# Kernel tuning notes

Measured on AMD Instinct MI355X. Metric: run time of the kernel, lower is better.

Reference implementation:

```python
import jax, jax.numpy as jnp
import numpy as np

D_MODEL = 1024
HEADS = 16
HEAD_DIM = D_MODEL // HEADS


def setup_inputs() -> dict:
    key = jax.random.key(0)
    ks = jax.random.split(key, 9)
    s = 1.0 / np.sqrt(D_MODEL)
    inp = {
        "inputs": jax.random.normal(ks[0], (4, 2048, D_MODEL), dtype=jnp.float32),
        "Wq": jax.random.normal(ks[1], (D_MODEL, D_MODEL), dtype=jnp.float32) * s,
        "bq": jnp.zeros((D_MODEL,), dtype=jnp.float32),
        "Wk": jax.random.normal(ks[2], (D_MODEL, D_MODEL), dtype=jnp.float32) * s,
        "bk": jnp.zeros((D_MODEL,), dtype=jnp.float32),
        "Wv": jax.random.normal(ks[3], (D_MODEL, D_MODEL), dtype=jnp.float32) * s,
        "bv": jnp.zeros((D_MODEL,), dtype=jnp.float32),
        "Wo": jax.random.normal(ks[4], (D_MODEL, D_MODEL), dtype=jnp.float32) * s,
        "bo": jnp.zeros((D_MODEL,), dtype=jnp.float32),
    }
    return inp


def reference(inputs, Wq, bq, Wk, bk, Wv, bv, Wo, bo):
    bs, seq, _ = inputs.shape
    # projections -> [b, h, s, d]
    def split_heads(x):
        return x.reshape(bs, seq, HEADS, HEAD_DIM).transpose(0, 2, 1, 3)
    q = split_heads(inputs @ Wq + bq)
    k = split_heads(inputs @ Wk + bk)
    v = split_heads(inputs @ Wv + bv)
    # NOTE: original code divides by (head_dim ** 1 / 2) == head_dim/2, not sqrt(head_dim)
    scale = HEAD_DIM / 2.0
    scores = jnp.einsum("bhqd,bhkd->bhqk", q, k) / scale
    attn = jax.nn.softmax(scores, axis=-1)
    out = jnp.einsum("bhqk,bhkd->bhqd", attn, v)
    out = out.transpose(0, 2, 1, 3).reshape(bs, seq, HEADS * HEAD_DIM)
    return out @ Wo + bo
```

## Files before the change

kernel.cpp:

```cpp
#include <hip/hip_runtime.h>
#include <stdint.h>

typedef __attribute__((ext_vector_type(8))) short bf16x8;
typedef __attribute__((ext_vector_type(4))) float f32x4;
typedef __attribute__((address_space(1))) void as1_void;
typedef __attribute__((address_space(3))) void as3_void;

#define D_MODEL 1024
#define SEQ     2048
#define BATCH   4
#define HEADS   16
#define HDIM    64

#define QSCALE 0.045084220029218407f

__device__ __forceinline__ ushort f2bf(float f) {
  union { float f; unsigned u; } v; v.f = f;
  unsigned u = v.u + 0x7fffu + ((v.u >> 16) & 1u);
  return (ushort)(u >> 16);
}

__device__ __forceinline__ void gload_lds16(const void* g, void* l) {
  __builtin_amdgcn_global_load_lds((as1_void*)(uintptr_t)g, (as3_void*)l, 16, 0, 0);
}

__device__ __forceinline__ bf16x8 pack8(float a0, float a1, float a2, float a3,
                                        float a4, float a5, float a6, float a7) {
  union { uint u[4]; bf16x8 v; } x;
  x.u[0] = __builtin_amdgcn_perm(__float_as_uint(a1), __float_as_uint(a0), 0x07060302);
  x.u[1] = __builtin_amdgcn_perm(__float_as_uint(a3), __float_as_uint(a2), 0x07060302);
  x.u[2] = __builtin_amdgcn_perm(__float_as_uint(a5), __float_as_uint(a4), 0x07060302);
  x.u[3] = __builtin_amdgcn_perm(__float_as_uint(a7), __float_as_uint(a6), 0x07060302);
  return x.v;
}

__global__ void prep_kernel(const float* __restrict__ X,
                            const float* w0, const float* w1, const float* w2, const float* w3,
                            const float* __restrict__ bq, const float* __restrict__ bk,
                            const float* __restrict__ bv,
                            ushort* __restrict__ Xb, ushort* __restrict__ WT,
                            float* __restrict__ bcat) {
  __shared__ float tile[32][33];
  const int bx = blockIdx.x, t = threadIdx.x;
  if (bx < 8192) {
    int i = bx * 256 + t;
    float4 f = reinterpret_cast<const float4*>(X)[i];
    ushort4 o;
    o.x = f2bf(f.x); o.y = f2bf(f.y); o.z = f2bf(f.z); o.w = f2bf(f.w);
    reinterpret_cast<ushort4*>(Xb)[i] = o;
  } else if (bx < 12288) {
    int tz = bx - 8192;
    int z = tz >> 10;
    int xy = tz & 1023;
    int bxt = xy & 31, byt = xy >> 5;
    const float* w = (z == 0) ? w0 : (z == 1) ? w1 : (z == 2) ? w2 : w3;
    const float sc = (z == 0) ? QSCALE : 1.0f;
    ushort* o = WT + (size_t)z * D_MODEL * D_MODEL;
    int tx = t & 31, ty = t >> 5;
    int x = bxt * 32 + tx;
    int y0 = byt * 32;
    #pragma unroll
    for (int i = ty; i < 32; i += 8)
      tile[i][tx] = w[(size_t)(y0 + i) * D_MODEL + x];
    __syncthreads();
    #pragma unroll
    for (int i = ty; i < 32; i += 8)
      o[(size_t)(bxt * 32 + i) * D_MODEL + y0 + tx] = f2bf(tile[tx][i] * sc);
  } else {
    int i = (bx - 12288) * 256 + t;
    bcat[i] = (i < 1024) ? bq[i] * QSCALE : (i < 2048) ? bk[i - 1024] : bv[i - 2048];
  }
}

#define MFMA16(a, b, c) __builtin_amdgcn_mfma_f32_16x16x32_bf16(a, b, c, 0, 0, 0)

template <int BN, bool F32OUT>
__global__ __launch_bounds__(256, 2) void gemm2p(const ushort* __restrict__ A,
                                                 const ushort* __restrict__ BT,
                                                 const float* __restrict__ bias,
                                                 ushort* __restrict__ QK,
                                                 ushort* __restrict__ Vt,
                                                 float* __restrict__ Cf) {
  static_assert(BN == 128, "gemm2p tuned for BN=128");
  constexpr int BB = BN * 128;
  __shared__ __align__(16) char smem[32768 + 2 * BB];
  const int tid  = threadIdx.x;
  const int w    = tid >> 6, lane = tid & 63;
  const int lo   = lane & 15, quad = lane >> 4;
  const int wr   = w >> 1, wc = w & 1;

  const int nx   = gridDim.x;
  const int nwg  = nx * gridDim.y;
  const int orig = blockIdx.y * nx + blockIdx.x;
  const int wg   = (orig & 7) * (nwg >> 3) + (orig >> 3);
  const int m0   = (wg / nx) * 128;
  const int n0   = (wg % nx) * BN;

  const int tl = tid ^ ((tid >> 3) & 7);
  const ushort* sA = A  + (size_t)(m0 + (tl >> 3)) * 1024 + (tl & 7) * 8;
  const ushort* sB = BT + (size_t)(n0 + (tl >> 3)) * 1024 + (tl & 7) * 8;
  char* lwA = smem + w * 1024;
  char* lwB = smem + 32768 + w * 1024;

  const int o0 = (quad * 16) ^ ((lo & 7) << 4);
  const int o1 = o0 ^ 64;
  const int rdA = (wr * 64 + lo) * 128;
  const int rdB = 32768 + (wc * 64 + lo) * 128;

  f32x4 acc[4][4];
  #pragma unroll
  for (int i = 0; i < 4; ++i)
    #pragma unroll
    for (int j = 0; j < 4; ++j) acc[i][j] = {0.f, 0.f, 0.f, 0.f};

  gload_lds16(sA,             lwA);
  gload_lds16(sA + 32 * 1024, lwA + 4096);
  gload_lds16(sA + 64 * 1024, lwA + 8192);
  gload_lds16(sA + 96 * 1024, lwA + 12288);
  gload_lds16(sB,             lwB);
  gload_lds16(sB + 64 * 1024, lwB + 8192);
  gload_lds16(sB + 32 * 1024, lwB + 4096);
  gload_lds16(sB + 96 * 1024, lwB + 12288);
  asm volatile("s_waitcnt vmcnt(2)" ::: "memory");
  __builtin_amdgcn_s_barrier();
  asm volatile("" ::: "memory");

  const char* L = smem;
  #pragma unroll 2
  for (int kt = 0; kt < 16; ++kt) {
    const int bA = (kt & 1) << 14;
    const int bB = (kt & 1) * BB;
    const int nA = bA ^ 16384;
    const int nB = bB ^ BB;
    const int kc = (kt + 1) * 64;
    const bool pf = kt < 15;
    bf16x8 af[4][2], bfr[2][2];

    #pragma unroll
    for (int mi = 0; mi < 4; ++mi) {
      af[mi][0] = *(const bf16x8*)(L + bA + rdA + mi * 2048 + o0);
      af[mi][1] = *(const bf16x8*)(L + bA + rdA + mi * 2048 + o1);
    }
    #pragma unroll
    for (int j = 0; j < 2; ++j) {
      bfr[j][0] = *(const bf16x8*)(L + bB + rdB + j * 2048 + o0);
      bfr[j][1] = *(const bf16x8*)(L + bB + rdB + j * 2048 + o1);
    }
    if (pf) {
      gload_lds16(sA + kc,             lwA + nA);
      gload_lds16(sA + 32 * 1024 + kc, lwA + nA + 4096);
      gload_lds16(sA + 64 * 1024 + kc, lwA + nA + 8192);
      gload_lds16(sA + 96 * 1024 + kc, lwA + nA + 12288);
      gload_lds16(sB + kc,             lwB + nB);
      gload_lds16(sB + 64 * 1024 + kc, lwB + nB + 8192);
    }
    asm volatile("s_waitcnt lgkmcnt(0)" ::: "memory");
    __builtin_amdgcn_sched_barrier(0);
    __builtin_amdgcn_s_setprio(1);
    #pragma unroll
    for (int ks = 0; ks < 2; ++ks)
      #pragma unroll
      for (int mi = 0; mi < 4; ++mi) {
        acc[mi][0] = MFMA16(af[mi][ks], bfr[0][ks], acc[mi][0]);
        acc[mi][1] = MFMA16(af[mi][ks], bfr[1][ks], acc[mi][1]);
      }
    __builtin_amdgcn_s_setprio(0);
    if (pf) asm volatile("s_waitcnt vmcnt(6)" ::: "memory");
    else    asm volatile("s_waitcnt vmcnt(0)" ::: "memory");
    __builtin_amdgcn_s_barrier();
    asm volatile("" ::: "memory");

    #pragma unroll
    for (int j = 0; j < 2; ++j) {
      bfr[j][0] = *(const bf16x8*)(L + bB + rdB + (2 + j) * 2048 + o0);
      bfr[j][1] = *(const bf16x8*)(L + bB + rdB + (2 + j) * 2048 + o1);
    }
    if (pf) {
      gload_lds16(sB + 32 * 1024 + kc, lwB + nB + 4096);
      gload_lds16(sB + 96 * 1024 + kc, lwB + nB + 12288);
    }
    asm volatile("s_waitcnt lgkmcnt(0)" ::: "memory");
    __builtin_amdgcn_sched_barrier(0);
    __builtin_amdgcn_s_setprio(1);
    #pragma unroll
    for (int ks = 0; ks < 2; ++ks)
      #pragma unroll
      for (int mi = 0; mi < 4; ++mi) {
        acc[mi][2] = MFMA16(af[mi][ks], bfr[0][ks], acc[mi][2]);
        acc[mi][3] = MFMA16(af[mi][ks], bfr[1][ks], acc[mi][3]);
      }
    __builtin_amdgcn_s_setprio(0);
    if (pf) {
      asm volatile("s_waitcnt vmcnt(2)" ::: "memory");
      __builtin_amdgcn_s_barrier();
      asm volatile("" ::: "memory");
    }
  }

  if constexpr (F32OUT) {
    #pragma unroll
    for (int ni = 0; ni < 4; ++ni) {
      const int col = n0 + wc * 64 + ni * 16 + lo;
      const float bv = bias[col];
      #pragma unroll
      for (int mi = 0; mi < 4; ++mi) {
        const int row = m0 + wr * 64 + mi * 16 + quad * 4;
        #pragma unroll
        for (int r = 0; r < 4; ++r)
          Cf[(size_t)(row + r) * 1024 + col] = acc[mi][ni][r] + bv;
      }
    }
  } else if (n0 < 2048) {
    #pragma unroll
    for (int ni = 0; ni < 4; ++ni) {
      const int col = n0 + wc * 64 + ni * 16 + lo;
      const float bv = bias[col];
      #pragma unroll
      for (int mi = 0; mi < 4; ++mi) {
        const int row = m0 + wr * 64 + mi * 16 + quad * 4;
        #pragma unroll
        for (int r = 0; r < 4; ++r)
          QK[(size_t)(row + r) * 2048 + col] = f2bf(acc[mi][ni][r] + bv);
      }
    }
  } else {
    #pragma unroll
    for (int ni = 0; ni < 4; ++ni) {
      const int col  = n0 + wc * 64 + ni * 16 + lo;
      const int vcol = col - 2048;
      const int hh = vcol >> 6, d = vcol & 63;
      const float bv = bias[col];
      #pragma unroll
      for (int mi = 0; mi < 4; ++mi) {
        const int base = m0 + wr * 64 + mi * 16;
        const int brow = base + quad * 4;
        const int bidx = brow >> 11;
        const int srow = brow & 2047;
        const int ck   = srow >> 6;
        const int c0   = (base & 32) + (quad << 3) + ((base >> 2) & 4);
        ushort e0 = f2bf(acc[mi][ni][0] + bv);
        ushort e1 = f2bf(acc[mi][ni][1] + bv);
        ushort e2 = f2bf(acc[mi][ni][2] + bv);
        ushort e3 = f2bf(acc[mi][ni][3] + bv);
        uint2 pk;
        pk.x = (uint)e0 | ((uint)e1 << 16);
        pk.y = (uint)e2 | ((uint)e3 << 16);
        *(uint2*)&Vt[(size_t)((bidx * HEADS + hh) * HDIM + d) * SEQ + ck * 64 + c0] = pk;
      }
    }
  }
}

__global__ __launch_bounds__(256, 2) void attn_kernel(const ushort* __restrict__ QK,
                                                      const ushort* __restrict__ Vt,
                                                      ushort* __restrict__ Og) {
  __shared__ __align__(16) ushort Ks[2][128 * 64];
  __shared__ __align__(16) ushort Vs[2][64 * 128];

  const int tid  = threadIdx.x;
  const int w    = tid >> 6, lane = tid & 63;
  const int lo   = lane & 15, quad = lane >> 4;

  const int p  = blockIdx.x + (blockIdx.y << 3) + (blockIdx.z << 7);
  const int G  = ((p >> 6) << 3) | (p & 7);
  const int h  = G & 15, b = G >> 4;
  const int qbase = ((p >> 3) & 7) * 256 + w * 64;
  const int swz = lo & 7;

  auto STAGE = [&](int buf, int ck) {
    #pragma unroll
    for (int i = 0; i < 4; ++i) {
      const int seg = w * 4 + i;
      const int c16 = seg * 64 + lane;
      const int rK = c16 >> 3, pK = c16 & 7;
      const int gK = pK ^ (rK & 7);
      gload_lds16(QK + (size_t)(b * SEQ + ck * 128 + rK) * 2048 + 1024 + h * HDIM + gK * 8,
                  &Ks[buf][seg * 512]);
      const int rV = c16 >> 4, pV = c16 & 15;
      const int gV = pV ^ (rV & 7);
      gload_lds16(Vt + (size_t)((b * HEADS + h) * HDIM + rV) * SEQ + ck * 128 + gV * 8,
                  &Vs[buf][seg * 512]);
    }
  };

  bf16x8 qf[4][2];
  #pragma unroll
  for (int qg = 0; qg < 4; ++qg) {
    const ushort* qp = QK + (size_t)(b * SEQ + qbase + qg * 16 + lo) * 2048 + h * HDIM;
    qf[qg][0] = *(const bf16x8*)(qp + quad * 8);
    qf[qg][1] = *(const bf16x8*)(qp + 32 + quad * 8);
  }

  bf16x8 ones;
  { union { uint u[4]; bf16x8 v; } o;
    o.u[0] = o.u[1] = o.u[2] = o.u[3] = 0x3F803F80u; ones = o.v; }

  f32x4 acc[4][4], acc_l[4];
  #pragma unroll
  for (int qg = 0; qg < 4; ++qg) {
    acc_l[qg] = {0.f, 0.f, 0.f, 0.f};
    #pragma unroll
    for (int t = 0; t < 4; ++t) acc[qg][t] = {0.f, 0.f, 0.f, 0.f};
  }

  STAGE(0, 0);
  __syncthreads();

  #pragma unroll 2
  for (int ck = 0; ck < SEQ / 128; ++ck) {
    const int cur = ck & 1;
    if (ck < SEQ / 128 - 1) {
      STAGE(cur ^ 1, ck + 1);
      asm volatile("s_waitcnt vmcnt(8)" ::: "memory");
    } else {
      asm volatile("s_waitcnt vmcnt(0)" ::: "memory");
    }
    __builtin_amdgcn_s_barrier();
    asm volatile("" ::: "memory");

    bf16x8 af[4][4];
    #pragma unroll
    for (int half = 0; half < 2; ++half) {
      bf16x8 kf[4][2];
      #pragma unroll
      for (int s2 = 0; s2 < 4; ++s2) {
        const ushort* kr = &Ks[cur][((half * 4 + s2) * 16 + lo) * 64];
        kf[s2][0] = *(const bf16x8*)(kr + ((quad ^ swz) * 8));
        kf[s2][1] = *(const bf16x8*)(kr + (((4 + quad) ^ swz) * 8));
      }
      #pragma unroll
      for (int qg = 0; qg < 4; ++qg) {
        f32x4 s[4];
        #pragma unroll
        for (int s2 = 0; s2 < 4; ++s2) s[s2] = {0.f, 0.f, 0.f, 0.f};
        #pragma unroll
        for (int s2 = 0; s2 < 4; ++s2) {
          s[s2] = MFMA16(kf[s2][0], qf[qg][0], s[s2]);
          s[s2] = MFMA16(kf[s2][1], qf[qg][1], s[s2]);
        }
        float p2[4][4];
        #pragma unroll
        for (int s2 = 0; s2 < 4; ++s2)
          #pragma unroll
          for (int r = 0; r < 4; ++r) p2[s2][r] = __builtin_amdgcn_exp2f(s[s2][r]);
        af[qg][half * 2 + 0] = pack8(p2[0][0], p2[0][1], p2[0][2], p2[0][3],
                                     p2[1][0], p2[1][1], p2[1][2], p2[1][3]);
        af[qg][half * 2 + 1] = pack8(p2[2][0], p2[2][1], p2[2][2], p2[2][3],
                                     p2[3][0], p2[3][1], p2[3][2], p2[3][3]);
      }
    }

    __builtin_amdgcn_s_setprio(1);
    #pragma unroll
    for (int qg = 0; qg < 4; ++qg)
      #pragma unroll
      for (int hh = 0; hh < 4; ++hh)
        acc_l[qg] = MFMA16(af[qg][hh], ones, acc_l[qg]);
    #pragma unroll
    for (int t = 0; t < 4; ++t) {
      const ushort* vr = &Vs[cur][(t * 16 + lo) * 128];
      #pragma unroll
      for (int hh = 0; hh < 4; ++hh) {
        bf16x8 vf = *(const bf16x8*)(vr + (((hh * 4 + quad) ^ swz) * 8));
        #pragma unroll
        for (int qg = 0; qg < 4; ++qg)
          acc[qg][t] = MFMA16(af[qg][hh], vf, acc[qg][t]);
      }
    }
    __builtin_amdgcn_s_setprio(0);

    asm volatile("" ::: "memory");
    __builtin_amdgcn_s_barrier();
    asm volatile("" ::: "memory");
  }

  #pragma unroll
  for (int qg = 0; qg < 4; ++qg) {
    float linv[4];
    #pragma unroll
    for (int r = 0; r < 4; ++r) linv[r] = 1.0f / acc_l[qg][r];
    #pragma unroll
    for (int t = 0; t < 4; ++t)
      #pragma unroll
      for (int r = 0; r < 4; ++r)
        Og[(size_t)(b * SEQ + qbase + qg * 16 + quad * 4 + r) * D_MODEL + h * HDIM + t * 16 + lo] =
            f2bf(acc[qg][t][r] * linv[r]);
  }
}

extern "C" void kernel_launch(void* const* d_in, const int* in_sizes, int n_in,
                              void* d_out, int out_size, void* d_ws, size_t ws_size,
                              hipStream_t stream) {
  const float* X  = (const float*)d_in[0];
  const float* Wq = (const float*)d_in[1];
  const float* bq = (const float*)d_in[2];
  const float* Wk = (const float*)d_in[3];
  const float* bk = (const float*)d_in[4];
  const float* Wv = (const float*)d_in[5];
  const float* bv = (const float*)d_in[6];
  const float* Wo = (const float*)d_in[7];
  const float* bo = (const float*)d_in[8];
  float* out = (float*)d_out;
  char* ws = (char*)d_ws;

  ushort* Xb  = (ushort*)(ws);
  ushort* WT  = (ushort*)(ws + 16777216);
  ushort* QKb = (ushort*)(ws + 25165824);
  ushort* Vtb = (ushort*)(ws + 58720256);
  ushort* Ob  = (ushort*)(ws + 75497472);
  float*  bcat = (float*)(ws + 75497472);
  const int WSTRIDE = D_MODEL * D_MODEL;

  prep_kernel<<<12300, 256, 0, stream>>>(X, Wq, Wk, Wv, Wo, bq, bk, bv, Xb, WT, bcat);

  gemm2p<128, false><<<dim3(24, 64), 256, 0, stream>>>(Xb, WT, bcat, QKb, Vtb, nullptr);

  attn_kernel<<<dim3(SEQ / 256, HEADS, BATCH), 256, 0, stream>>>(QKb, Vtb, Ob);

  gemm2p<128, true><<<dim3(8, 64), 256, 0, stream>>>(Ob, WT + 3 * WSTRIDE, bo, nullptr, nullptr, out);
}
```

Measured before the change: 241.2 us.

## Software-pipeline attention halves so PV of previous half overlaps next QK/exp

Splits each 128-key chunk of the attention loop into two 64-key halves and interleaves them across iterations. The P·V MFMAs of the previous chunk's second half run alongside the QK and exp2 work of the current chunk, so exp/VALU work can overlap matrix work. V is staged into three rotating 64x64-half buffers so the delayed PV still has its data. The change adds LDS use (K double buffer plus a V triple buffer), a prologue and epilogue, drops the setprio hints and the unroll-2 pragma, and may raise register pressure.

Measured after the change: 252.1 us. 4.6% more time.

```diff
diff --git a/kernel.cpp b/kernel.cpp
--- a/kernel.cpp
+++ b/kernel.cpp
@@ -254,8 +254,8 @@
 __global__ __launch_bounds__(256, 2) void attn_kernel(const ushort* __restrict__ QK,
                                                       const ushort* __restrict__ Vt,
                                                       ushort* __restrict__ Og) {
-  __shared__ __align__(16) ushort Ks[2][128 * 64];
-  __shared__ __align__(16) ushort Vs[2][64 * 128];
+  __shared__ __align__(16) ushort KsL[2 * 128 * 64];
+  __shared__ __align__(16) ushort VsL[3 * 2 * 64 * 64];
 
   const int tid  = threadIdx.x;
   const int w    = tid >> 6, lane = tid & 63;
@@ -267,7 +267,7 @@
   const int qbase = ((p >> 3) & 7) * 256 + w * 64;
   const int swz = lo & 7;
 
-  auto STAGE = [&](int buf, int ck) {
+  auto STAGE = [&](int kb, int vb, int ck) {
     #pragma unroll
     for (int i = 0; i < 4; ++i) {
       const int seg = w * 4 + i;
@@ -275,11 +275,13 @@
       const int rK = c16 >> 3, pK = c16 & 7;
       const int gK = pK ^ (rK & 7);
       gload_lds16(QK + (size_t)(b * SEQ + ck * 128 + rK) * 2048 + 1024 + h * HDIM + gK * 8,
-                  &Ks[buf][seg * 512]);
-      const int rV = c16 >> 4, pV = c16 & 15;
-      const int gV = pV ^ (rV & 7);
-      gload_lds16(Vt + (size_t)((b * HEADS + h) * HDIM + rV) * SEQ + ck * 128 + gV * 8,
-                  &Vs[buf][seg * 512]);
+                  &KsL[kb * 8192 + seg * 512]);
+      const int half = seg >> 3;
+      const int d = (seg & 7) * 8 + (lane >> 3);
+      const int pV = lane & 7;
+      const int gV = pV ^ (d & 7);
+      gload_lds16(Vt + (size_t)((b * HEADS + h) * HDIM + d) * SEQ + ck * 128 + half * 64 + gV * 8,
+                  &VsL[vb * 8192 + seg * 512]);
     }
   };
 
@@ -303,14 +305,78 @@
     for (int t = 0; t < 4; ++t) acc[qg][t] = {0.f, 0.f, 0.f, 0.f};
   }
 
-  STAGE(0, 0);
+  auto HALF = [&](bf16x8 (&afo)[4][2], int kb, int half) {
+    const ushort* kbase = &KsL[kb * 8192];
+    bf16x8 kf[4][2];
+    #pragma unroll
+    for (int s2 = 0; s2 < 4; ++s2) {
+      const ushort* kr = kbase + ((half * 4 + s2) * 16 + lo) * 64;
+      kf[s2][0] = *(const bf16x8*)(kr + ((quad ^ swz) * 8));
+      kf[s2][1] = *(const bf16x8*)(kr + (((4 + quad) ^ swz) * 8));
+    }
+    #pragma unroll
+    for (int qg = 0; qg < 4; ++qg) {
+      f32x4 s[4];
+      #pragma unroll
+      for (int s2 = 0; s2 < 4; ++s2) s[s2] = {0.f, 0.f, 0.f, 0.f};
+      #pragma unroll
+      for (int s2 = 0; s2 < 4; ++s2) {
+        s[s2] = MFMA16(kf[s2][0], qf[qg][0], s[s2]);
+        s[s2] = MFMA16(kf[s2][1], qf[qg][1], s[s2]);
+      }
+      float p2[4][4];
+      #pragma unroll
+      for (int s2 = 0; s2 < 4; ++s2)
+        #pragma unroll
+        for (int r = 0; r < 4; ++r) p2[s2][r] = __builtin_amdgcn_exp2f(s[s2][r]);
+      afo[qg][0] = pack8(p2[0][0], p2[0][1], p2[0][2], p2[0][3],
+                         p2[1][0], p2[1][1], p2[1][2], p2[1][3]);
+      afo[qg][1] = pack8(p2[2][0], p2[2][1], p2[2][2], p2[2][3],
+                         p2[3][0], p2[3][1], p2[3][2], p2[3][3]);
+    }
+  };
+
+  auto PVH = [&](bf16x8 (&afp)[4][2], int vb, int halfV) {
+    #pragma unroll
+    for (int qg = 0; qg < 4; ++qg)
+      #pragma unroll
+      for (int j = 0; j < 2; ++j)
+        acc_l[qg] = MFMA16(afp[qg][j], ones, acc_l[qg]);
+    const ushort* vbase = &VsL[vb * 8192 + halfV * 4096];
+    #pragma unroll
+    for (int t = 0; t < 4; ++t) {
+      const ushort* vrh = vbase + (t * 16 + lo) * 64;
+      #pragma unroll
+      for (int j = 0; j < 2; ++j) {
+        bf16x8 vf = *(const bf16x8*)(vrh + (((j * 4 + quad) ^ swz) * 8));
+        #pragma unroll
+        for (int qg = 0; qg < 4; ++qg)
+          acc[qg][t] = MFMA16(afp[qg][j], vf, acc[qg][t]);
+      }
+    }
+  };
+
+  bf16x8 afA[4][2], afB[4][2];
+
+  STAGE(0, 0, 0);
   __syncthreads();
 
-  #pragma unroll 2
-  for (int ck = 0; ck < SEQ / 128; ++ck) {
-    const int cur = ck & 1;
+  STAGE(1, 1, 1);
+  asm volatile("s_waitcnt vmcnt(8)" ::: "memory");
+  __builtin_amdgcn_s_barrier();
+  asm volatile("" ::: "memory");
+  HALF(afA, 0, 0);
+  HALF(afB, 0, 1);
+  PVH(afA, 0, 0);
+  asm volatile("" ::: "memory");
+  __builtin_amdgcn_s_barrier();
+  asm volatile("" ::: "memory");
+
+  int vprev = 0, vcur = 1, vnext = 2;
+  for (int ck = 1; ck < SEQ / 128; ++ck) {
+    const int kb = ck & 1;
     if (ck < SEQ / 128 - 1) {
-      STAGE(cur ^ 1, ck + 1);
+      STAGE(kb ^ 1, vnext, ck + 1);
       asm volatile("s_waitcnt vmcnt(8)" ::: "memory");
     } else {
       asm volatile("s_waitcnt vmcnt(0)" ::: "memory");
@@ -318,61 +384,19 @@
     __builtin_amdgcn_s_barrier();
     asm volatile("" ::: "memory");
 
-    bf16x8 af[4][4];
-    #pragma unroll
-    for (int half = 0; half < 2; ++half) {
-      bf16x8 kf[4][2];
-      #pragma unroll
-      for (int s2 = 0; s2 < 4; ++s2) {
-        const ushort* kr = &Ks[cur][((half * 4 + s2) * 16 + lo) * 64];
-        kf[s2][0] = *(const bf16x8*)(kr + ((quad ^ swz) * 8));
-        kf[s2][1] = *(const bf16x8*)(kr + (((4 + quad) ^ swz) * 8));
-      }
-      #pragma unroll
-      for (int qg = 0; qg < 4; ++qg) {
-        f32x4 s[4];
-        #pragma unroll
-        for (int s2 = 0; s2 < 4; ++s2) s[s2] = {0.f, 0.f, 0.f, 0.f};
-        #pragma unroll
-        for (int s2 = 0; s2 < 4; ++s2) {
-          s[s2] = MFMA16(kf[s2][0], qf[qg][0], s[s2]);
-          s[s2] = MFMA16(kf[s2][1], qf[qg][1], s[s2]);
-        }
-        float p2[4][4];
-        #pragma unroll
-        for (int s2 = 0; s2 < 4; ++s2)
-          #pragma unroll
-          for (int r = 0; r < 4; ++r) p2[s2][r] = __builtin_amdgcn_exp2f(s[s2][r]);
-        af[qg][half * 2 + 0] = pack8(p2[0][0], p2[0][1], p2[0][2], p2[0][3],
-                                     p2[1][0], p2[1][1], p2[1][2], p2[1][3]);
-        af[qg][half * 2 + 1] = pack8(p2[2][0], p2[2][1], p2[2][2], p2[2][3],
-                                     p2[3][0], p2[3][1], p2[3][2], p2[3][3]);
-      }
-    }
-
-    __builtin_amdgcn_s_setprio(1);
-    #pragma unroll
-    for (int qg = 0; qg < 4; ++qg)
-      #pragma unroll
-      for (int hh = 0; hh < 4; ++hh)
-        acc_l[qg] = MFMA16(af[qg][hh], ones, acc_l[qg]);
-    #pragma unroll
-    for (int t = 0; t < 4; ++t) {
-      const ushort* vr = &Vs[cur][(t * 16 + lo) * 128];
-      #pragma unroll
-      for (int hh = 0; hh < 4; ++hh) {
-        bf16x8 vf = *(const bf16x8*)(vr + (((hh * 4 + quad) ^ swz) * 8));
-        #pragma unroll
-        for (int qg = 0; qg < 4; ++qg)
-          acc[qg][t] = MFMA16(af[qg][hh], vf, acc[qg][t]);
-      }
-    }
-    __builtin_amdgcn_s_setprio(0);
+    HALF(afA, kb, 0);
+    PVH(afB, vprev, 1);
+    HALF(afB, kb, 1);
+    PVH(afA, vcur, 0);
 
     asm volatile("" ::: "memory");
     __builtin_amdgcn_s_barrier();
     asm volatile("" ::: "memory");
-  }
+
+    const int t0 = vprev; vprev = vcur; vcur = vnext; vnext = t0;
+  }
+
+  PVH(afB, vprev, 1);
 
   #pragma unroll
   for (int qg = 0; qg < 4; ++qg) {
```

## Use 8 waves per attention block with 32 query rows each and per-half PV

Applied to the files above, without the earlier changes.

The attention kernel now runs 512 threads per block, each wave owning 32 query rows instead of 64, so the K/V tiles staged in LDS are shared by twice as many waves. The V tile is re-laid out as two 64-key halves, which lets each half's probabilities be consumed by the PV MFMAs right away instead of holding all of them in registers. This lowers per-thread register pressure and raises occupancy (launch bounds 512,4), and the s_setprio hints are dropped. In exchange each wave issues fewer MFMAs per LDS K/V fragment read, and the changed staging pattern and wait counts have to be correct.

Result: slower. 248.6 us (+3.1%).

```diff
diff --git a/kernel.cpp b/kernel.cpp
--- a/kernel.cpp
+++ b/kernel.cpp
@@ -251,11 +251,11 @@
   }
 }
 
-__global__ __launch_bounds__(256, 2) void attn_kernel(const ushort* __restrict__ QK,
+__global__ __launch_bounds__(512, 4) void attn_kernel(const ushort* __restrict__ QK,
                                                       const ushort* __restrict__ Vt,
                                                       ushort* __restrict__ Og) {
   __shared__ __align__(16) ushort Ks[2][128 * 64];
-  __shared__ __align__(16) ushort Vs[2][64 * 128];
+  __shared__ __align__(16) ushort Vs[2][2 * 64 * 64];
 
   const int tid  = threadIdx.x;
   const int w    = tid >> 6, lane = tid & 63;
@@ -264,28 +264,30 @@
   const int p  = blockIdx.x + (blockIdx.y << 3) + (blockIdx.z << 7);
   const int G  = ((p >> 6) << 3) | (p & 7);
   const int h  = G & 15, b = G >> 4;
-  const int qbase = ((p >> 3) & 7) * 256 + w * 64;
+  const int qbase = ((p >> 3) & 7) * 256 + w * 32;
   const int swz = lo & 7;
 
   auto STAGE = [&](int buf, int ck) {
     #pragma unroll
-    for (int i = 0; i < 4; ++i) {
-      const int seg = w * 4 + i;
+    for (int i = 0; i < 2; ++i) {
+      const int seg = w * 2 + i;
       const int c16 = seg * 64 + lane;
       const int rK = c16 >> 3, pK = c16 & 7;
       const int gK = pK ^ (rK & 7);
       gload_lds16(QK + (size_t)(b * SEQ + ck * 128 + rK) * 2048 + 1024 + h * HDIM + gK * 8,
                   &Ks[buf][seg * 512]);
-      const int rV = c16 >> 4, pV = c16 & 15;
-      const int gV = pV ^ (rV & 7);
-      gload_lds16(Vt + (size_t)((b * HEADS + h) * HDIM + rV) * SEQ + ck * 128 + gV * 8,
+      const int half = seg >> 3;
+      const int d = (seg & 7) * 8 + (lane >> 3);
+      const int pV = lane & 7;
+      const int gV = pV ^ (d & 7);
+      gload_lds16(Vt + (size_t)((b * HEADS + h) * HDIM + d) * SEQ + ck * 128 + half * 64 + gV * 8,
                   &Vs[buf][seg * 512]);
     }
   };
 
-  bf16x8 qf[4][2];
+  bf16x8 qf[2][2];
   #pragma unroll
-  for (int qg = 0; qg < 4; ++qg) {
+  for (int qg = 0; qg < 2; ++qg) {
     const ushort* qp = QK + (size_t)(b * SEQ + qbase + qg * 16 + lo) * 2048 + h * HDIM;
     qf[qg][0] = *(const bf16x8*)(qp + quad * 8);
     qf[qg][1] = *(const bf16x8*)(qp + 32 + quad * 8);
@@ -295,9 +297,9 @@
   { union { uint u[4]; bf16x8 v; } o;
     o.u[0] = o.u[1] = o.u[2] = o.u[3] = 0x3F803F80u; ones = o.v; }
 
-  f32x4 acc[4][4], acc_l[4];
+  f32x4 acc[2][4], acc_l[2];
   #pragma unroll
-  for (int qg = 0; qg < 4; ++qg) {
+  for (int qg = 0; qg < 2; ++qg) {
     acc_l[qg] = {0.f, 0.f, 0.f, 0.f};
     #pragma unroll
     for (int t = 0; t < 4; ++t) acc[qg][t] = {0.f, 0.f, 0.f, 0.f};
@@ -311,14 +313,13 @@
     const int cur = ck & 1;
     if (ck < SEQ / 128 - 1) {
       STAGE(cur ^ 1, ck + 1);
-      asm volatile("s_waitcnt vmcnt(8)" ::: "memory");
+      asm volatile("s_waitcnt vmcnt(4)" ::: "memory");
     } else {
       asm volatile("s_waitcnt vmcnt(0)" ::: "memory");
     }
     __builtin_amdgcn_s_barrier();
     asm volatile("" ::: "memory");
 
-    bf16x8 af[4][4];
     #pragma unroll
     for (int half = 0; half < 2; ++half) {
       bf16x8 kf[4][2];
@@ -328,8 +329,9 @@
         kf[s2][0] = *(const bf16x8*)(kr + ((quad ^ swz) * 8));
         kf[s2][1] = *(const bf16x8*)(kr + (((4 + quad) ^ swz) * 8));
       }
-      #pragma unroll
-      for (int qg = 0; qg < 4; ++qg) {
+      bf16x8 af[2][2];
+      #pragma unroll
+      for (int qg = 0; qg < 2; ++qg) {
         f32x4 s[4];
         #pragma unroll
         for (int s2 = 0; s2 < 4; ++s2) s[s2] = {0.f, 0.f, 0.f, 0.f};
@@ -343,31 +345,30 @@
         for (int s2 = 0; s2 < 4; ++s2)
           #pragma unroll
           for (int r = 0; r < 4; ++r) p2[s2][r] = __builtin_amdgcn_exp2f(s[s2][r]);
-        af[qg][half * 2 + 0] = pack8(p2[0][0], p2[0][1], p2[0][2], p2[0][3],
-                                     p2[1][0], p2[1][1], p2[1][2], p2[1][3]);
-        af[qg][half * 2 + 1] = pack8(p2[2][0], p2[2][1], p2[2][2], p2[2][3],
-                                     p2[3][0], p2[3][1], p2[3][2], p2[3][3]);
-      }
-    }
-
-    __builtin_amdgcn_s_setprio(1);
-    #pragma unroll
-    for (int qg = 0; qg < 4; ++qg)
-      #pragma unroll
-      for (int hh = 0; hh < 4; ++hh)
-        acc_l[qg] = MFMA16(af[qg][hh], ones, acc_l[qg]);
-    #pragma unroll
-    for (int t = 0; t < 4; ++t) {
-      const ushort* vr = &Vs[cur][(t * 16 + lo) * 128];
-      #pragma unroll
-      for (int hh = 0; hh < 4; ++hh) {
-        bf16x8 vf = *(const bf16x8*)(vr + (((hh * 4 + quad) ^ swz) * 8));
-        #pragma unroll
-        for (int qg = 0; qg < 4; ++qg)
-          acc[qg][t] = MFMA16(af[qg][hh], vf, acc[qg][t]);
-      }
-    }
-    __builtin_amdgcn_s_setprio(0);
+        af[qg][0] = pack8(p2[0][0], p2[0][1], p2[0][2], p2[0][3],
+                          p2[1][0], p2[1][1], p2[1][2], p2[1][3]);
+        af[qg][1] = pack8(p2[2][0], p2[2][1], p2[2][2], p2[2][3],
+                          p2[3][0], p2[3][1], p2[3][2], p2[3][3]);
+      }
+
+      #pragma unroll
+      for (int qg = 0; qg < 2; ++qg) {
+        acc_l[qg] = MFMA16(af[qg][0], ones, acc_l[qg]);
+        acc_l[qg] = MFMA16(af[qg][1], ones, acc_l[qg]);
+      }
+      const ushort* vbase = &Vs[cur][half * 4096];
+      #pragma unroll
+      for (int t = 0; t < 4; ++t) {
+        const ushort* vrh = vbase + (t * 16 + lo) * 64;
+        #pragma unroll
+        for (int j = 0; j < 2; ++j) {
+          bf16x8 vf = *(const bf16x8*)(vrh + (((j * 4 + quad) ^ swz) * 8));
+          #pragma unroll
+          for (int qg = 0; qg < 2; ++qg)
+            acc[qg][t] = MFMA16(af[qg][j], vf, acc[qg][t]);
+        }
+      }
+    }
 
     asm volatile("" ::: "memory");
     __builtin_amdgcn_s_barrier();
@@ -375,7 +376,7 @@
   }
 
   #pragma unroll
-  for (int qg = 0; qg < 4; ++qg) {
+  for (int qg = 0; qg < 2; ++qg) {
     float linv[4];
     #pragma unroll
     for (int r = 0; r < 4; ++r) linv[r] = 1.0f / acc_l[qg][r];
@@ -415,7 +416,7 @@
 
   gemm2p<128, false><<<dim3(24, 64), 256, 0, stream>>>(Xb, WT, bcat, QKb, Vtb, nullptr);
 
-  attn_kernel<<<dim3(SEQ / 256, HEADS, BATCH), 256, 0, stream>>>(QKb, Vtb, Ob);
+  attn_kernel<<<dim3(8, 16, 4), 512, 0, stream>>>(QKb, Vtb, Ob);
 
   gemm2p<128, true><<<dim3(8, 64), 256, 0, stream>>>(Ob, WT + 3 * WSTRIDE, bo, nullptr, nullptr, out);
 }
```
